# Kernel optimization log

Hardware: AMD Instinct MI355X
Metric: run time of the kernel (lower is better)

## Reference

```python
import jax, jax.numpy as jnp
import numpy as np

TEMPERATURE = 0.5
EPS = 1e-12  # matches F.normalize eps


def setup_inputs() -> dict:
    key = jax.random.key(0)
    k1, k2 = jax.random.split(key)
    B, D = 4096, 128
    z_i = jax.random.normal(k1, (B, D), dtype=jnp.float32)
    z_j = jax.random.normal(k2, (B, D), dtype=jnp.float32)
    return {"z_i": z_i, "z_j": z_j}


def _l2_normalize(x):
    # F.normalize(x, dim=1): x / max(||x||, eps)
    norm = jnp.sqrt(jnp.sum(x * x, axis=1, keepdims=True))
    return x / jnp.maximum(norm, EPS)


def reference(z_i, z_j):
    B = z_i.shape[0]
    zi = _l2_normalize(z_i)
    zj = _l2_normalize(z_j)
    z = jnp.concatenate([zi, zj], axis=0)  # [2B, D], rows unit-norm
    # cosine similarity of unit vectors == dot product
    sim = jnp.matmul(z, z.T) / TEMPERATURE  # [2B, 2B]
    # Removing the diagonal and shifting columns (as in the torch code) is
    # equivalent, for cross-entropy, to masking the diagonal with -inf: the
    # diagonal contributes exp(-inf)=0 to logsumexp and labels never hit it.
    n = 2 * B
    diag = jnp.eye(n, dtype=bool)
    logits = jnp.where(diag, -jnp.inf, sim)
    # positive for row i (<B) is column i+B; for row i+B it is column i
    ar = jnp.arange(B)
    labels = jnp.concatenate([ar + B, ar])  # indices in the FULL matrix
    lse = jax.nn.logsumexp(logits, axis=1)  # [2B]
    pos = sim[jnp.arange(n), labels]  # positive logits (never on diag)
    loss = jnp.sum(lse - pos) / n
    return loss
```

## Files before the change

kernel.cpp:

```cpp
#include <hip/hip_runtime.h>
#include <hip/hip_bf16.h>
#include <math.h>

#define B_ROWS 4096
#define N_ROWS 8192
#define D 128
#define EXP2_SCALE 2.8853900817779268f
#define LN2F 0.6931471805599453f
#define NT 32
#define NBLK 528
#define NSLOT 32
#define TS 256

#define AS1 __attribute__((address_space(1)))
#define AS3 __attribute__((address_space(3)))

typedef __attribute__((ext_vector_type(8))) short bf16x8;
typedef __attribute__((ext_vector_type(4))) float f32x4;

#define MFMA(A, B, C) __builtin_amdgcn_mfma_f32_16x16x32_bf16(A, B, C, 0, 0, 0)

__global__ __launch_bounds__(256) void normalize_kernel(
    const float* __restrict__ z_i, const float* __restrict__ z_j,
    ushort* __restrict__ Zu, ushort* __restrict__ Zs) {
  const int wave = threadIdx.x >> 6;
  const int lane = threadIdx.x & 63;
  const int row = blockIdx.x * 4 + wave;
  const float* src = (row < B_ROWS) ? (z_i + (size_t)row * D)
                                    : (z_j + (size_t)(row - B_ROWS) * D);
  float2 v = *(const float2*)(src + lane * 2);
  float ss = v.x * v.x + v.y * v.y;
#pragma unroll
  for (int off = 32; off > 0; off >>= 1) ss += __shfl_xor(ss, off);
  float scale = 1.0f / fmaxf(sqrtf(ss), 1e-12f);
  float u0 = v.x * scale, u1 = v.y * scale;
  __hip_bfloat16 h0 = __float2bfloat16(u0);
  __hip_bfloat16 h1 = __float2bfloat16(u1);
  __hip_bfloat16 g0 = __float2bfloat16(u0 * EXP2_SCALE);
  __hip_bfloat16 g1 = __float2bfloat16(u1 * EXP2_SCALE);
  ushort2 ou, os;
  ou.x = *(ushort*)&h0; ou.y = *(ushort*)&h1;
  os.x = *(ushort*)&g0; os.y = *(ushort*)&g1;
  *(ushort2*)(Zu + (size_t)row * D + lane * 2) = ou;
  *(ushort2*)(Zs + (size_t)row * D + lane * 2) = os;
}

__global__ __launch_bounds__(512) void sim_kernel(
    const ushort* __restrict__ Zu, const ushort* __restrict__ Zs,
    float* __restrict__ partials, float* __restrict__ pos_buf) {
  __shared__ ushort ldsB[TS * 128];
  __shared__ float colpart[8][TS];

  int idx = (int)(blockIdx.x % 8) * (NBLK / 8) + (int)(blockIdx.x / 8);
  int I = (int)(32.5f - sqrtf(32.5f * 32.5f - 2.0f * (float)idx));
  if (I < 0) I = 0;
  if (I > NT - 1) I = NT - 1;
  while ((I + 1) * NT - ((I + 1) * I) / 2 <= idx) ++I;
  while (I * NT - (I * (I - 1)) / 2 > idx) --I;
  const int J = I + (idx - (I * NT - (I * (I - 1)) / 2));
  const int rI = I * TS, rJ = J * TS;
  const bool DIAG = (I == J);
  const bool POS = (J == I + 16);

  const int t = threadIdx.x;
  const int lane = t & 63;
  const int w = t >> 6;
  const int l15 = lane & 15;
  const int l4 = lane >> 4;

  const ushort* Abase = Zu + (size_t)(rI + w * 32 + l15) * D + l4 * 8;
  const bf16x8 a00 = *(const bf16x8*)(Abase);
  const bf16x8 a01 = *(const bf16x8*)(Abase + 32);
  const bf16x8 a02 = *(const bf16x8*)(Abase + 64);
  const bf16x8 a03 = *(const bf16x8*)(Abase + 96);
  const bf16x8 a10 = *(const bf16x8*)(Abase + 16 * D);
  const bf16x8 a11 = *(const bf16x8*)(Abase + 16 * D + 32);
  const bf16x8 a12 = *(const bf16x8*)(Abase + 16 * D + 64);
  const bf16x8 a13 = *(const bf16x8*)(Abase + 16 * D + 96);

  {
    const int rsub = lane >> 4;
#pragma unroll
    for (int i = 0; i < 8; ++i) {
      const int row = i * 32 + w * 4 + rsub;
      const int srcoff = ((lane & 15) * 16) ^ ((row & 7) << 4);
      const char* src = (const char*)Zs + (size_t)(rJ + row) * 256 + srcoff;
      char* dst = (char*)ldsB + (size_t)(i * 32 + w * 4) * 256;
      __builtin_amdgcn_global_load_lds((AS1 const unsigned int*)src,
                                       (AS3 unsigned int*)dst, 16, 0, 0);
    }
  }
  __syncthreads();

  f32x4 rsum0 = {0.f, 0.f, 0.f, 0.f};
  f32x4 rsum1 = {0.f, 0.f, 0.f, 0.f};

#pragma unroll 4
  for (int cs = 0; cs < 16; ++cs) {
    const int br = cs * 16 + l15;
    const int bo = br * 256, bsw = (br & 7) << 4;
    bf16x8 b0 = *(const bf16x8*)((const char*)ldsB + bo + ((0 + l4 * 16) ^ bsw));
    bf16x8 b1 = *(const bf16x8*)((const char*)ldsB + bo + ((64 + l4 * 16) ^ bsw));
    bf16x8 b2 = *(const bf16x8*)((const char*)ldsB + bo + ((128 + l4 * 16) ^ bsw));
    bf16x8 b3 = *(const bf16x8*)((const char*)ldsB + bo + ((192 + l4 * 16) ^ bsw));
    f32x4 c0 = {0.f, 0.f, 0.f, 0.f};
    f32x4 c1 = {0.f, 0.f, 0.f, 0.f};
    c0 = MFMA(a00, b0, c0); c1 = MFMA(a10, b0, c1);
    c0 = MFMA(a01, b1, c0); c1 = MFMA(a11, b1, c1);
    c0 = MFMA(a02, b2, c0); c1 = MFMA(a12, b2, c1);
    c0 = MFMA(a03, b3, c0); c1 = MFMA(a13, b3, c1);

    const int bt = cs * 16 + l15;
    float cp = 0.f;
    if (!DIAG && !POS) {
#pragma unroll
      for (int r = 0; r < 4; ++r) {
        float e0 = __builtin_amdgcn_exp2f(c0[r]);
        float e1 = __builtin_amdgcn_exp2f(c1[r]);
        rsum0[r] += e0;
        rsum1[r] += e1;
        cp += e0 + e1;
      }
    } else if (DIAG) {
#pragma unroll
      for (int r = 0; r < 4; ++r) {
        const int at0 = w * 32 + l4 * 4 + r;
        const int at1 = at0 + 16;
        float e0 = __builtin_amdgcn_exp2f(c0[r]);
        float e1 = __builtin_amdgcn_exp2f(c1[r]);
        rsum0[r] += (at0 != bt) ? e0 : 0.f;
        rsum1[r] += (at1 != bt) ? e1 : 0.f;
      }
    } else {
#pragma unroll
      for (int r = 0; r < 4; ++r) {
        const int at0 = w * 32 + l4 * 4 + r;
        const int at1 = at0 + 16;
        float e0 = __builtin_amdgcn_exp2f(c0[r]);
        float e1 = __builtin_amdgcn_exp2f(c1[r]);
        if (at0 == bt) { pos_buf[rI + at0] = c0[r]; pos_buf[rJ + at0] = c0[r]; }
        if (at1 == bt) { pos_buf[rI + at1] = c1[r]; pos_buf[rJ + at1] = c1[r]; }
        rsum0[r] += e0;
        rsum1[r] += e1;
        cp += e0 + e1;
      }
    }
    cp += __shfl_xor(cp, 16);
    cp += __shfl_xor(cp, 32);
    if (l4 == 0) colpart[w][bt] = cp;
  }

#pragma unroll
  for (int r = 0; r < 4; ++r) {
    float v0 = rsum0[r], v1 = rsum1[r];
    v0 += __shfl_xor(v0, 1); v0 += __shfl_xor(v0, 2);
    v0 += __shfl_xor(v0, 4); v0 += __shfl_xor(v0, 8);
    v1 += __shfl_xor(v1, 1); v1 += __shfl_xor(v1, 2);
    v1 += __shfl_xor(v1, 4); v1 += __shfl_xor(v1, 8);
    rsum0[r] = v0; rsum1[r] = v1;
  }
  if (l15 == 0) {
    *(f32x4*)&partials[(size_t)J * N_ROWS + rI + w * 32 + l4 * 4] = rsum0;
    *(f32x4*)&partials[(size_t)J * N_ROWS + rI + w * 32 + 16 + l4 * 4] = rsum1;
  }

  __syncthreads();
  if (!DIAG && t < TS) {
    float v = colpart[0][t] + colpart[1][t] + colpart[2][t] + colpart[3][t] +
              colpart[4][t] + colpart[5][t] + colpart[6][t] + colpart[7][t];
    partials[(size_t)I * N_ROWS + rJ + t] = v;
  }
}

__global__ __launch_bounds__(256) void reduce1_kernel(
    const float* __restrict__ partials, const float* __restrict__ pos_buf,
    float* __restrict__ loss_part) {
  const int row = blockIdx.x * 256 + threadIdx.x;
  float tot = 0.f;
#pragma unroll 8
  for (int s = 0; s < NSLOT; ++s) tot += partials[(size_t)s * N_ROWS + row];
  float term = (log2f(tot) - pos_buf[row]) * LN2F;
#pragma unroll
  for (int off = 32; off > 0; off >>= 1) term += __shfl_xor(term, off);
  __shared__ float wsum[4];
  if ((threadIdx.x & 63) == 0) wsum[threadIdx.x >> 6] = term;
  __syncthreads();
  if (threadIdx.x == 0)
    loss_part[blockIdx.x] = wsum[0] + wsum[1] + wsum[2] + wsum[3];
}

__global__ __launch_bounds__(64) void reduce2_kernel(
    const float* __restrict__ loss_part, float* __restrict__ out) {
  float v = (threadIdx.x < 32) ? loss_part[threadIdx.x] : 0.f;
#pragma unroll
  for (int off = 32; off > 0; off >>= 1) v += __shfl_xor(v, off);
  if (threadIdx.x == 0) out[0] = v / (float)N_ROWS;
}

extern "C" void kernel_launch(void* const* d_in, const int* in_sizes, int n_in,
                              void* d_out, int out_size, void* d_ws, size_t ws_size,
                              hipStream_t stream) {
  const float* z_i = (const float*)d_in[0];
  const float* z_j = (const float*)d_in[1];
  float* out = (float*)d_out;

  ushort* Zu = (ushort*)d_ws;
  ushort* Zs = Zu + (size_t)N_ROWS * D;
  float* partials = (float*)(Zs + (size_t)N_ROWS * D);
  float* pos_buf = partials + (size_t)NSLOT * N_ROWS;
  float* loss_part = pos_buf + N_ROWS;

  hipLaunchKernelGGL(normalize_kernel, dim3(N_ROWS / 4), dim3(256), 0, stream,
                     z_i, z_j, Zu, Zs);
  hipLaunchKernelGGL(sim_kernel, dim3(NBLK), dim3(512), 0, stream, Zu, Zs,
                     partials, pos_buf);
  hipLaunchKernelGGL(reduce1_kernel, dim3(N_ROWS / 256), dim3(256), 0, stream,
                     partials, pos_buf, loss_part);
  hipLaunchKernelGGL(reduce2_kernel, dim3(1), dim3(64), 0, stream, loss_part,
                     out);
}
```

Baseline: 83.26 us.

## Merge scaled normalized matrices into one and fuse final reduction via atomic counter

Both GEMM operands are scaled by the square root of the exp2 temperature factor so one bf16 matrix serves as both A and B, halving normalize writes. The final reduction kernel is folded into reduce1 using an atomic ticket counter so the last block sums the partials, removing a kernel launch. Both operands are now rounded after scaling, which slightly changes rounding, and the design relies on the counter reset done in normalize.

```diff
diff --git a/kernel.cpp b/kernel.cpp
--- a/kernel.cpp
+++ b/kernel.cpp
@@ -5,7 +5,7 @@
 #define B_ROWS 4096
 #define N_ROWS 8192
 #define D 128
-#define EXP2_SCALE 2.8853900817779268f
+#define SQRT_SCALE 1.6986436f
 #define LN2F 0.6931471805599453f
 #define NT 32
 #define NBLK 528
@@ -22,7 +22,8 @@
 
 __global__ __launch_bounds__(256) void normalize_kernel(
     const float* __restrict__ z_i, const float* __restrict__ z_j,
-    ushort* __restrict__ Zu, ushort* __restrict__ Zs) {
+    ushort* __restrict__ Z, unsigned int* __restrict__ sync_cnt) {
+  if (blockIdx.x == 0 && threadIdx.x == 0) sync_cnt[0] = 0u;
   const int wave = threadIdx.x >> 6;
   const int lane = threadIdx.x & 63;
   const int row = blockIdx.x * 4 + wave;
@@ -32,22 +33,17 @@
   float ss = v.x * v.x + v.y * v.y;
 #pragma unroll
   for (int off = 32; off > 0; off >>= 1) ss += __shfl_xor(ss, off);
-  float scale = 1.0f / fmaxf(sqrtf(ss), 1e-12f);
-  float u0 = v.x * scale, u1 = v.y * scale;
-  __hip_bfloat16 h0 = __float2bfloat16(u0);
-  __hip_bfloat16 h1 = __float2bfloat16(u1);
-  __hip_bfloat16 g0 = __float2bfloat16(u0 * EXP2_SCALE);
-  __hip_bfloat16 g1 = __float2bfloat16(u1 * EXP2_SCALE);
-  ushort2 ou, os;
-  ou.x = *(ushort*)&h0; ou.y = *(ushort*)&h1;
+  float scale = SQRT_SCALE / fmaxf(sqrtf(ss), 1e-12f);
+  __hip_bfloat16 g0 = __float2bfloat16(v.x * scale);
+  __hip_bfloat16 g1 = __float2bfloat16(v.y * scale);
+  ushort2 os;
   os.x = *(ushort*)&g0; os.y = *(ushort*)&g1;
-  *(ushort2*)(Zu + (size_t)row * D + lane * 2) = ou;
-  *(ushort2*)(Zs + (size_t)row * D + lane * 2) = os;
+  *(ushort2*)(Z + (size_t)row * D + lane * 2) = os;
 }
 
 __global__ __launch_bounds__(512) void sim_kernel(
-    const ushort* __restrict__ Zu, const ushort* __restrict__ Zs,
-    float* __restrict__ partials, float* __restrict__ pos_buf) {
+    const ushort* __restrict__ Z, float* __restrict__ partials,
+    float* __restrict__ pos_buf) {
   __shared__ ushort ldsB[TS * 128];
   __shared__ float colpart[8][TS];
 
@@ -68,7 +64,7 @@
   const int l15 = lane & 15;
   const int l4 = lane >> 4;
 
-  const ushort* Abase = Zu + (size_t)(rI + w * 32 + l15) * D + l4 * 8;
+  const ushort* Abase = Z + (size_t)(rI + w * 32 + l15) * D + l4 * 8;
   const bf16x8 a00 = *(const bf16x8*)(Abase);
   const bf16x8 a01 = *(const bf16x8*)(Abase + 32);
   const bf16x8 a02 = *(const bf16x8*)(Abase + 64);
@@ -84,7 +80,7 @@
     for (int i = 0; i < 8; ++i) {
       const int row = i * 32 + w * 4 + rsub;
       const int srcoff = ((lane & 15) * 16) ^ ((row & 7) << 4);
-      const char* src = (const char*)Zs + (size_t)(rJ + row) * 256 + srcoff;
+      const char* src = (const char*)Z + (size_t)(rJ + row) * 256 + srcoff;
       char* dst = (char*)ldsB + (size_t)(i * 32 + w * 4) * 256;
       __builtin_amdgcn_global_load_lds((AS1 const unsigned int*)src,
                                        (AS3 unsigned int*)dst, 16, 0, 0);
@@ -174,7 +170,8 @@
 
 __global__ __launch_bounds__(256) void reduce1_kernel(
     const float* __restrict__ partials, const float* __restrict__ pos_buf,
-    float* __restrict__ loss_part) {
+    float* __restrict__ loss_part, unsigned int* __restrict__ sync_cnt,
+    float* __restrict__ out) {
   const int row = blockIdx.x * 256 + threadIdx.x;
   float tot = 0.f;
 #pragma unroll 8
@@ -183,18 +180,27 @@
 #pragma unroll
   for (int off = 32; off > 0; off >>= 1) term += __shfl_xor(term, off);
   __shared__ float wsum[4];
+  __shared__ unsigned int is_last;
   if ((threadIdx.x & 63) == 0) wsum[threadIdx.x >> 6] = term;
   __syncthreads();
-  if (threadIdx.x == 0)
-    loss_part[blockIdx.x] = wsum[0] + wsum[1] + wsum[2] + wsum[3];
-}
-
-__global__ __launch_bounds__(64) void reduce2_kernel(
-    const float* __restrict__ loss_part, float* __restrict__ out) {
-  float v = (threadIdx.x < 32) ? loss_part[threadIdx.x] : 0.f;
-#pragma unroll
-  for (int off = 32; off > 0; off >>= 1) v += __shfl_xor(v, off);
-  if (threadIdx.x == 0) out[0] = v / (float)N_ROWS;
+  if (threadIdx.x == 0) {
+    float bsum = wsum[0] + wsum[1] + wsum[2] + wsum[3];
+    __hip_atomic_store(&loss_part[blockIdx.x], bsum, __ATOMIC_RELEASE,
+                       __HIP_MEMORY_SCOPE_AGENT);
+    unsigned int old = __hip_atomic_fetch_add(sync_cnt, 1u, __ATOMIC_ACQ_REL,
+                                              __HIP_MEMORY_SCOPE_AGENT);
+    is_last = (old == (N_ROWS / 256) - 1) ? 1u : 0u;
+  }
+  __syncthreads();
+  if (is_last && threadIdx.x < 64) {
+    float v = (threadIdx.x < 32)
+                  ? __hip_atomic_load(&loss_part[threadIdx.x], __ATOMIC_ACQUIRE,
+                                      __HIP_MEMORY_SCOPE_AGENT)
+                  : 0.f;
+#pragma unroll
+    for (int off = 32; off > 0; off >>= 1) v += __shfl_xor(v, off);
+    if (threadIdx.x == 0) out[0] = v / (float)N_ROWS;
+  }
 }
 
 extern "C" void kernel_launch(void* const* d_in, const int* in_sizes, int n_in,
@@ -204,18 +210,16 @@
   const float* z_j = (const float*)d_in[1];
   float* out = (float*)d_out;
 
-  ushort* Zu = (ushort*)d_ws;
-  ushort* Zs = Zu + (size_t)N_ROWS * D;
-  float* partials = (float*)(Zs + (size_t)N_ROWS * D);
+  ushort* Z = (ushort*)d_ws;
+  float* partials = (float*)(Z + (size_t)N_ROWS * D);
   float* pos_buf = partials + (size_t)NSLOT * N_ROWS;
   float* loss_part = pos_buf + N_ROWS;
+  unsigned int* sync_cnt = (unsigned int*)(loss_part + 32);
 
   hipLaunchKernelGGL(normalize_kernel, dim3(N_ROWS / 4), dim3(256), 0, stream,
-                     z_i, z_j, Zu, Zs);
-  hipLaunchKernelGGL(sim_kernel, dim3(NBLK), dim3(512), 0, stream, Zu, Zs,
-                     partials, pos_buf);
+                     z_i, z_j, Z, sync_cnt);
+  hipLaunchKernelGGL(sim_kernel, dim3(NBLK), dim3(512), 0, stream, Z, partials,
+                     pos_buf);
   hipLaunchKernelGGL(reduce1_kernel, dim3(N_ROWS / 256), dim3(256), 0, stream,
-                     partials, pos_buf, loss_part);
-  hipLaunchKernelGGL(reduce2_kernel, dim3(1), dim3(64), 0, stream, loss_part,
-                     out);
-}
+                     partials, pos_buf, loss_part, sync_cnt, out);
+}
```

Result: slower. 84.96 us (+2.0%).
